# Optimization experiments

Hardware: AMD Instinct MI355X
Metric: run time of the kernel (lower is better)

The kernel has to match this reference:

```python
import jax, jax.numpy as jnp
import numpy as np

N, C, NELL, NSPEC = 4096, 128, 9, 10
K3, K2, K1 = 4, 2, 1
IRREPS_OUT = (("0e", 1), ("1o", 3))  # keep_irrep_out dims


def setup_inputs() -> dict:
    key = jax.random.key(0)
    ks = iter(jax.random.split(key, 32))

    def rn(shape, scale=1.0):
        return jax.random.normal(next(ks), shape, jnp.float32) * jnp.float32(scale)

    inp = {}
    inp["x"] = rn((N, C, NELL))
    inp["node_specie"] = jax.random.randint(next(ks), (N,), 0, NSPEC)
    for name, d in IRREPS_OUT:
        # CG symmetric-product basis tensors (fixed buffers), normalized per order
        inp[f"U3_{name}"] = rn((d, NELL, NELL, NELL, K3), 1.0 / np.sqrt(NELL ** 3))
        inp[f"U2_{name}"] = rn((d, NELL, NELL, K2), 1.0 / np.sqrt(NELL ** 2))
        inp[f"U1_{name}"] = rn((d, NELL, K1), 1.0 / np.sqrt(NELL))
        # per-species path-mixing weights, 'element' gradient normalization ~ 1/sqrt(k)
        inp[f"W3_{name}"] = rn((NSPEC, K3, C), 1.0 / np.sqrt(K3))
        inp[f"W2_{name}"] = rn((NSPEC, K2, C), 1.0 / np.sqrt(K2))
        inp[f"W1_{name}"] = rn((NSPEC, K1, C), 1.0 / np.sqrt(K1))
    inp["Wlin_0e"] = rn((C, C))
    inp["Wlin_1o"] = rn((C, C))
    inp["bias_0e"] = rn((C,), 0.1)
    return inp


def _symmetric_contraction(x, specie, U3, U2, U1, W3, W2, W1):
    # MACE iterative contraction: out = U3.W3.x; then (U2.W2 + out).x; then (U1.W1 + out).x
    w3, w2, w1 = W3[specie], W2[specie], W1[specie]  # (N, k, C)
    out = jnp.einsum("opqik,bkc,bci->bcopq", U3, w3, x)   # (N, C, d, 9, 9)
    c = jnp.einsum("opik,bkc->bcopi", U2, w2) + out
    out = jnp.einsum("bcopi,bci->bcop", c, x)             # (N, C, d, 9)
    c = jnp.einsum("oik,bkc->bcoi", U1, w1) + out
    out = jnp.einsum("bcoi,bci->bco", c, x)               # (N, C, d)
    return out


def reference(x, node_specie,
              U3_0e, U2_0e, U1_0e, W3_0e, W2_0e, W1_0e,
              U3_1o, U2_1o, U1_1o, W3_1o, W2_1o, W1_1o,
              Wlin_0e, Wlin_1o, bias_0e):
    n = x.shape[0]
    f0 = _symmetric_contraction(x, node_specie, U3_0e, U2_0e, U1_0e, W3_0e, W2_0e, W1_0e)  # (N, C, 1)
    f1 = _symmetric_contraction(x, node_specie, U3_1o, U2_1o, U1_1o, W3_1o, W2_1o, W1_1o)  # (N, C, 3)
    scale = jnp.float32(1.0 / np.sqrt(C))  # e3nn Linear path normalization
    y0 = jnp.einsum("nco,cm->nmo", f0, Wlin_0e) * scale + bias_0e[None, :, None]  # bias only on 0e
    y1 = jnp.einsum("nco,cm->nmo", f1, Wlin_1o) * scale
    # axis_to_mul: flatten (channels, ir_dim) per irrep and concatenate
    return jnp.concatenate([y0.reshape(n, -1), y1.reshape(n, -1)], axis=-1)  # (N, 128*1 + 128*3)
```

## Files before the change

### kernel.cpp

```cpp
#include <hip/hip_runtime.h>

#define N_NODES 4096
#define C_CH    128
#define NSPEC   10
#define NCUB    165
#define NQUAD   45
#define NMONO   219
#define NBLK    1280
#define NTILE   8

#define WS_CNT    0
#define WS_LIST   256
#define WS_U3SYM  164096
#define WS_U2SYM  174656
#define WS_COEFF  176096
#define WS_F      4661216

__global__ void k_prep(const float* __restrict__ U3_0e, const float* __restrict__ U3_1o,
                       const float* __restrict__ U2_0e, const float* __restrict__ U2_1o,
                       int* __restrict__ cnt, float* __restrict__ U3sym,
                       float* __restrict__ U2sym) {
    __shared__ unsigned char ta[NCUB], tb[NCUB], td[NCUB], qa[NQUAD], qb[NQUAD];
    int t = threadIdx.x;
    if (t < NSPEC) cnt[t] = 0;
    if (t < NCUB) {
        int idx = 0, a = 0, b = 0, d = 0;
        for (int a0 = 0; a0 < 9; a0++)
            for (int b0 = a0; b0 < 9; b0++)
                for (int d0 = b0; d0 < 9; d0++) {
                    if (idx == t) { a = a0; b = b0; d = d0; }
                    idx++;
                }
        ta[t] = a; tb[t] = b; td[t] = d;
    } else if (t >= 256 && t < 256 + NQUAD) {
        int q = t - 256, idx = 0, a = 0, b = 0;
        for (int a0 = 0; a0 < 9; a0++)
            for (int b0 = a0; b0 < 9; b0++) { if (idx == q) { a = a0; b = b0; } idx++; }
        qa[q] = a; qb[q] = b;
    }
    __syncthreads();
    for (int task = t; task < 2640 + 360; task += blockDim.x) {
        if (task < 2640) {
            int og = task / 660;
            int r  = task - og * 660;
            int m  = r >> 2, k = r & 3;
            int a = ta[m], b = tb[m], d = td[m];
            const float* U3 = (og == 0) ? U3_0e : U3_1o;
            int o = (og == 0) ? 0 : og - 1;
            const float* Ub = U3 + (size_t)o * 2916;
            #define U3AT(p,q,i) Ub[((p)*9+(q))*36 + (i)*4 + k]
            float sum = U3AT(a,b,d) + U3AT(a,d,b) + U3AT(b,a,d)
                      + U3AT(b,d,a) + U3AT(d,a,b) + U3AT(d,b,a);
            #undef U3AT
            float sc = (a == b && b == d) ? (1.f/6.f)
                     : ((a == b || b == d || a == d) ? 0.5f : 1.f);
            U3sym[(og * 165 + m) * 4 + k] = sum * sc;
        } else {
            int t2 = task - 2640;
            int og = t2 / 90;
            int r  = t2 - og * 90;
            int q  = r >> 1, k = r & 1;
            int a = qa[q], b = qb[q];
            const float* U2 = (og == 0) ? U2_0e : U2_1o;
            int o = (og == 0) ? 0 : og - 1;
            const float* Ub = U2 + (size_t)o * 162;
            float sum = Ub[(a*9 + b)*2 + k] + Ub[(b*9 + a)*2 + k];
            if (a == b) sum *= 0.5f;
            U2sym[(og * 45 + q) * 2 + k] = sum;
        }
    }
}

__global__ void k_lists(const int* __restrict__ specie, int* __restrict__ cnt,
                        int* __restrict__ list) {
    int i = blockIdx.x * blockDim.x + threadIdx.x;
    if (i < N_NODES) {
        int s = specie[i];
        int pos = atomicAdd(&cnt[s], 1);
        list[s * N_NODES + pos] = i;
    }
}

__global__ void k_coeff(const float* __restrict__ U3sym, const float* __restrict__ U2sym,
                        const float* __restrict__ U1_0e, const float* __restrict__ U1_1o,
                        const float* __restrict__ W3_0e, const float* __restrict__ W3_1o,
                        const float* __restrict__ W2_0e, const float* __restrict__ W2_1o,
                        const float* __restrict__ W1_0e, const float* __restrict__ W1_1o,
                        float* __restrict__ coeff) {
    int blk = blockIdx.x;
    int s = blk >> 7, c = blk & 127;
    int t = threadIdx.x;
    if (t >= NMONO * 4) return;
    int m = t >> 2, og = t & 3;
    float val;
    if (m < NCUB) {
        const float* W3 = (og == 0) ? W3_0e : W3_1o;
        const float* u  = U3sym + (og * 165 + m) * 4;
        val = u[0] * W3[s*512 +       c] + u[1] * W3[s*512 + 128 + c]
            + u[2] * W3[s*512 + 256 + c] + u[3] * W3[s*512 + 384 + c];
    } else if (m < NCUB + NQUAD) {
        int q = m - NCUB;
        const float* W2 = (og == 0) ? W2_0e : W2_1o;
        const float* u  = U2sym + (og * 45 + q) * 2;
        val = u[0] * W2[s*256 + c] + u[1] * W2[s*256 + 128 + c];
    } else {
        int l = m - (NCUB + NQUAD);
        const float* U1 = (og == 0) ? U1_0e : U1_1o;
        const float* W1 = (og == 0) ? W1_0e : W1_1o;
        int o = (og == 0) ? 0 : og - 1;
        val = U1[o * 9 + l] * W1[s * 128 + c];
    }
    coeff[(size_t)blk * (NMONO * 4) + t] = val;
}

__global__ __launch_bounds__(256) void k_main(const float* __restrict__ x,
        const int* __restrict__ cnt, const int* __restrict__ list,
        const float* __restrict__ coeff, float* __restrict__ fout) {
    __shared__ float  cfs[NMONO * 4];
    __shared__ float2 xsh[9 * 256];
    int bx   = blockIdx.x;
    int tile = bx / NBLK;
    int blk  = bx - tile * NBLK;
    int s = blk >> 7, c = blk & 127;
    int n = cnt[s];
    if (tile * 512 >= n) return;

    int tid = threadIdx.x;
    if (tid < NMONO)
        ((float4*)cfs)[tid] =
            ((const float4*)(coeff + (size_t)blk * (NMONO * 4)))[tid];

    const int* __restrict__ lst = list + s * N_NODES;
    int i0 = tile * 512 + tid;
    int i1 = i0 + 256;
    int b0 = lst[i0 < n ? i0 : 0];
    int b1 = lst[i1 < n ? i1 : 0];
    const float* xp0 = x + ((size_t)b0 * C_CH + c) * 9;
    const float* xp1 = x + ((size_t)b1 * C_CH + c) * 9;
    #pragma unroll
    for (int i = 0; i < 9; i++)
        xsh[i * 256 + tid] = make_float2(xp0[i], xp1[i]);
    __syncthreads();

    float a0[4] = {0.f, 0.f, 0.f, 0.f};
    float a1[4] = {0.f, 0.f, 0.f, 0.f};
    int mcub = 0, mquad = 0;

    #pragma unroll 1
    for (int a = 0; a < 9; a++) {
        float2 xa = xsh[a * 256 + tid];
        {
            float4 cl = *(const float4*)&cfs[(210 + a) * 4];
            a0[0] = fmaf(cl.x, xa.x, a0[0]);  a1[0] = fmaf(cl.x, xa.y, a1[0]);
            a0[1] = fmaf(cl.y, xa.x, a0[1]);  a1[1] = fmaf(cl.y, xa.y, a1[1]);
            a0[2] = fmaf(cl.z, xa.x, a0[2]);  a1[2] = fmaf(cl.z, xa.y, a1[2]);
            a0[3] = fmaf(cl.w, xa.x, a0[3]);  a1[3] = fmaf(cl.w, xa.y, a1[3]);
        }
        #pragma unroll 1
        for (int b = a; b < 9; b++) {
            float2 xb = xsh[b * 256 + tid];
            float p0 = xa.x * xb.x, p1 = xa.y * xb.y;
            {
                float4 cq = *(const float4*)&cfs[(165 + mquad) * 4]; mquad++;
                a0[0] = fmaf(cq.x, p0, a0[0]);  a1[0] = fmaf(cq.x, p1, a1[0]);
                a0[1] = fmaf(cq.y, p0, a0[1]);  a1[1] = fmaf(cq.y, p1, a1[1]);
                a0[2] = fmaf(cq.z, p0, a0[2]);  a1[2] = fmaf(cq.z, p1, a1[2]);
                a0[3] = fmaf(cq.w, p0, a0[3]);  a1[3] = fmaf(cq.w, p1, a1[3]);
            }
            #pragma unroll 1
            for (int d = b; d < 9; d++) {
                float2 xd = xsh[d * 256 + tid];
                float4 c3 = *(const float4*)&cfs[mcub * 4]; mcub++;
                float q0 = p0 * xd.x, q1 = p1 * xd.y;
                a0[0] = fmaf(c3.x, q0, a0[0]);  a1[0] = fmaf(c3.x, q1, a1[0]);
                a0[1] = fmaf(c3.y, q0, a0[1]);  a1[1] = fmaf(c3.y, q1, a1[1]);
                a0[2] = fmaf(c3.z, q0, a0[2]);  a1[2] = fmaf(c3.z, q1, a1[2]);
                a0[3] = fmaf(c3.w, q0, a0[3]);  a1[3] = fmaf(c3.w, q1, a1[3]);
            }
        }
    }
    if (i0 < n) *(float4*)&fout[((size_t)b0 * C_CH + c) * 4] = make_float4(a0[0], a0[1], a0[2], a0[3]);
    if (i1 < n) *(float4*)&fout[((size_t)b1 * C_CH + c) * 4] = make_float4(a1[0], a1[1], a1[2], a1[3]);
}

__global__ __launch_bounds__(256) void k_epi(const float* __restrict__ f,
        const float* __restrict__ W0, const float* __restrict__ W1,
        const float* __restrict__ bias, float* __restrict__ out) {
    __shared__ float smem[128 * 65];
    int bx = blockIdx.x;
    int ntile = bx >> 3, jg = bx & 7;
    int n0 = ntile * 64;
    int t  = threadIdx.x;
    int o  = jg >> 1;

    #pragma unroll
    for (int r = 0; r < 32; ++r) {
        int flat = r * 256 + t;
        int n = flat >> 7, c = flat & 127;
        smem[c * 65 + n] = f[(size_t)(n0 + n) * 512 + c * 4 + o];
    }
    __syncthreads();

    int w    = __builtin_amdgcn_readfirstlane((int)(t >> 6));
    int lane = t & 63;
    int mb   = (jg & 1) * 64 + w * 16;
    const float* __restrict__ Wsel = (o == 0) ? W0 : W1;

    float acc[16];
    #pragma unroll
    for (int jj = 0; jj < 16; jj++) acc[jj] = 0.f;

    #pragma unroll 4
    for (int c = 0; c < 128; ++c) {
        float fv = smem[c * 65 + lane];
        #pragma unroll
        for (int jj = 0; jj < 16; jj++)
            acc[jj] = fmaf(fv, Wsel[c * 128 + mb + jj], acc[jj]);
    }
    __syncthreads();

    const float scale = 0.08838834764831845f;
    #pragma unroll
    for (int jj = 0; jj < 16; jj++) {
        float v = acc[jj] * scale;
        if (o == 0) v += bias[mb + jj];
        smem[(w * 16 + jj) * 65 + lane] = v;
    }
    __syncthreads();

    #pragma unroll
    for (int r = 0; r < 16; ++r) {
        int flat = r * 256 + t;
        int jl = flat & 63, n = flat >> 6;
        int m  = (jg & 1) * 64 + jl;
        int col = (o == 0) ? m : (128 + m * 3 + (o - 1));
        out[(size_t)(n0 + n) * 512 + col] = smem[jl * 65 + n];
    }
}

extern "C" void kernel_launch(void* const* d_in, const int* in_sizes, int n_in,
                              void* d_out, int out_size, void* d_ws, size_t ws_size,
                              hipStream_t stream) {
    const float* x     = (const float*)d_in[0];
    const int*   spec  = (const int*)  d_in[1];
    const float* U3_0e = (const float*)d_in[2];
    const float* U2_0e = (const float*)d_in[3];
    const float* U1_0e = (const float*)d_in[4];
    const float* W3_0e = (const float*)d_in[5];
    const float* W2_0e = (const float*)d_in[6];
    const float* W1_0e = (const float*)d_in[7];
    const float* U3_1o = (const float*)d_in[8];
    const float* U2_1o = (const float*)d_in[9];
    const float* U1_1o = (const float*)d_in[10];
    const float* W3_1o = (const float*)d_in[11];
    const float* W2_1o = (const float*)d_in[12];
    const float* W1_1o = (const float*)d_in[13];
    const float* Wlin0 = (const float*)d_in[14];
    const float* Wlin1 = (const float*)d_in[15];
    const float* bias0 = (const float*)d_in[16];
    float* out = (float*)d_out;

    char* ws = (char*)d_ws;
    int*   cnt   = (int*)  (ws + WS_CNT);
    int*   list  = (int*)  (ws + WS_LIST);
    float* U3sym = (float*)(ws + WS_U3SYM);
    float* U2sym = (float*)(ws + WS_U2SYM);
    float* coeff = (float*)(ws + WS_COEFF);
    float* f     = (float*)(ws + WS_F);
    (void)in_sizes; (void)n_in; (void)out_size; (void)ws_size;

    hipLaunchKernelGGL(k_prep,  dim3(1),    dim3(1024), 0, stream,
                       U3_0e, U3_1o, U2_0e, U2_1o, cnt, U3sym, U2sym);
    hipLaunchKernelGGL(k_lists, dim3(16),   dim3(256),  0, stream, spec, cnt, list);
    hipLaunchKernelGGL(k_coeff, dim3(1280), dim3(896),  0, stream,
                       U3sym, U2sym, U1_0e, U1_1o, W3_0e, W3_1o,
                       W2_0e, W2_1o, W1_0e, W1_1o, coeff);
    hipLaunchKernelGGL(k_main,  dim3(NBLK * NTILE), dim3(256), 0, stream,
                       x, cnt, list, coeff, f);
    hipLaunchKernelGGL(k_epi,   dim3(512),  dim3(256),  0, stream, f, Wlin0, Wlin1, bias0, out);
}
```

Baseline: 185.2 us.

## Fuse list building into prep and compute coefficients inside main kernel

Merges the species-list kernel into a multi-block prep kernel: one block builds the per-species node lists with shared-memory atomics, and eight blocks compute the symmetrized U tensors. The per-(species, channel) coefficient kernel and its workspace buffer are removed, and k_main now computes its 876 coefficients directly into shared memory. This drops two launches and a roughly 4.5 MB coefficient write and read-back. In exchange, every main block, including tiles that are only partly filled, recomputes its coefficients from global U and W buffers.

```diff
diff --git a/kernel.cpp b/kernel.cpp
--- a/kernel.cpp
+++ b/kernel.cpp
@@ -13,16 +13,32 @@
 #define WS_LIST   256
 #define WS_U3SYM  164096
 #define WS_U2SYM  174656
-#define WS_COEFF  176096
-#define WS_F      4661216
-
-__global__ void k_prep(const float* __restrict__ U3_0e, const float* __restrict__ U3_1o,
-                       const float* __restrict__ U2_0e, const float* __restrict__ U2_1o,
-                       int* __restrict__ cnt, float* __restrict__ U3sym,
-                       float* __restrict__ U2sym) {
+#define WS_F      176096
+
+__global__ __launch_bounds__(256) void k_prep(
+        const float* __restrict__ U3_0e, const float* __restrict__ U3_1o,
+        const float* __restrict__ U2_0e, const float* __restrict__ U2_1o,
+        const int* __restrict__ specie, int* __restrict__ cnt,
+        int* __restrict__ list, float* __restrict__ U3sym,
+        float* __restrict__ U2sym) {
+    int blk = blockIdx.x;
+    int t   = threadIdx.x;
+
+    if (blk == 8) {
+        __shared__ int scnt[NSPEC];
+        if (t < NSPEC) scnt[t] = 0;
+        __syncthreads();
+        for (int i = t; i < N_NODES; i += 256) {
+            int s = specie[i];
+            int pos = atomicAdd(&scnt[s], 1);
+            list[s * N_NODES + pos] = i;
+        }
+        __syncthreads();
+        if (t < NSPEC) cnt[t] = scnt[t];
+        return;
+    }
+
     __shared__ unsigned char ta[NCUB], tb[NCUB], td[NCUB], qa[NQUAD], qb[NQUAD];
-    int t = threadIdx.x;
-    if (t < NSPEC) cnt[t] = 0;
     if (t < NCUB) {
         int idx = 0, a = 0, b = 0, d = 0;
         for (int a0 = 0; a0 < 9; a0++)
@@ -32,14 +48,15 @@
                     idx++;
                 }
         ta[t] = a; tb[t] = b; td[t] = d;
-    } else if (t >= 256 && t < 256 + NQUAD) {
-        int q = t - 256, idx = 0, a = 0, b = 0;
+    } else if (t >= NCUB && t < NCUB + NQUAD) {
+        int q = t - NCUB, idx = 0, a = 0, b = 0;
         for (int a0 = 0; a0 < 9; a0++)
             for (int b0 = a0; b0 < 9; b0++) { if (idx == q) { a = a0; b = b0; } idx++; }
         qa[q] = a; qb[q] = b;
     }
     __syncthreads();
-    for (int task = t; task < 2640 + 360; task += blockDim.x) {
+
+    for (int task = blk * 256 + t; task < 2640 + 360; task += 8 * 256) {
         if (task < 2640) {
             int og = task / 660;
             int r  = task - og * 660;
@@ -71,51 +88,14 @@
     }
 }
 
-__global__ void k_lists(const int* __restrict__ specie, int* __restrict__ cnt,
-                        int* __restrict__ list) {
-    int i = blockIdx.x * blockDim.x + threadIdx.x;
-    if (i < N_NODES) {
-        int s = specie[i];
-        int pos = atomicAdd(&cnt[s], 1);
-        list[s * N_NODES + pos] = i;
-    }
-}
-
-__global__ void k_coeff(const float* __restrict__ U3sym, const float* __restrict__ U2sym,
-                        const float* __restrict__ U1_0e, const float* __restrict__ U1_1o,
-                        const float* __restrict__ W3_0e, const float* __restrict__ W3_1o,
-                        const float* __restrict__ W2_0e, const float* __restrict__ W2_1o,
-                        const float* __restrict__ W1_0e, const float* __restrict__ W1_1o,
-                        float* __restrict__ coeff) {
-    int blk = blockIdx.x;
-    int s = blk >> 7, c = blk & 127;
-    int t = threadIdx.x;
-    if (t >= NMONO * 4) return;
-    int m = t >> 2, og = t & 3;
-    float val;
-    if (m < NCUB) {
-        const float* W3 = (og == 0) ? W3_0e : W3_1o;
-        const float* u  = U3sym + (og * 165 + m) * 4;
-        val = u[0] * W3[s*512 +       c] + u[1] * W3[s*512 + 128 + c]
-            + u[2] * W3[s*512 + 256 + c] + u[3] * W3[s*512 + 384 + c];
-    } else if (m < NCUB + NQUAD) {
-        int q = m - NCUB;
-        const float* W2 = (og == 0) ? W2_0e : W2_1o;
-        const float* u  = U2sym + (og * 45 + q) * 2;
-        val = u[0] * W2[s*256 + c] + u[1] * W2[s*256 + 128 + c];
-    } else {
-        int l = m - (NCUB + NQUAD);
-        const float* U1 = (og == 0) ? U1_0e : U1_1o;
-        const float* W1 = (og == 0) ? W1_0e : W1_1o;
-        int o = (og == 0) ? 0 : og - 1;
-        val = U1[o * 9 + l] * W1[s * 128 + c];
-    }
-    coeff[(size_t)blk * (NMONO * 4) + t] = val;
-}
-
 __global__ __launch_bounds__(256) void k_main(const float* __restrict__ x,
         const int* __restrict__ cnt, const int* __restrict__ list,
-        const float* __restrict__ coeff, float* __restrict__ fout) {
+        const float* __restrict__ U3sym, const float* __restrict__ U2sym,
+        const float* __restrict__ U1_0e, const float* __restrict__ U1_1o,
+        const float* __restrict__ W3_0e, const float* __restrict__ W3_1o,
+        const float* __restrict__ W2_0e, const float* __restrict__ W2_1o,
+        const float* __restrict__ W1_0e, const float* __restrict__ W1_1o,
+        float* __restrict__ fout) {
     __shared__ float  cfs[NMONO * 4];
     __shared__ float2 xsh[9 * 256];
     int bx   = blockIdx.x;
@@ -126,9 +106,29 @@
     if (tile * 512 >= n) return;
 
     int tid = threadIdx.x;
-    if (tid < NMONO)
-        ((float4*)cfs)[tid] =
-            ((const float4*)(coeff + (size_t)blk * (NMONO * 4)))[tid];
+
+    for (int e = tid; e < NMONO * 4; e += 256) {
+        int m = e >> 2, og = e & 3;
+        float val;
+        if (m < NCUB) {
+            const float* W3 = (og == 0) ? W3_0e : W3_1o;
+            const float* u  = U3sym + (og * 165 + m) * 4;
+            val = u[0] * W3[s*512 +       c] + u[1] * W3[s*512 + 128 + c]
+                + u[2] * W3[s*512 + 256 + c] + u[3] * W3[s*512 + 384 + c];
+        } else if (m < NCUB + NQUAD) {
+            int q = m - NCUB;
+            const float* W2 = (og == 0) ? W2_0e : W2_1o;
+            const float* u  = U2sym + (og * 45 + q) * 2;
+            val = u[0] * W2[s*256 + c] + u[1] * W2[s*256 + 128 + c];
+        } else {
+            int l = m - (NCUB + NQUAD);
+            const float* U1 = (og == 0) ? U1_0e : U1_1o;
+            const float* W1 = (og == 0) ? W1_0e : W1_1o;
+            int o = (og == 0) ? 0 : og - 1;
+            val = U1[o * 9 + l] * W1[s * 128 + c];
+        }
+        cfs[e] = val;
+    }
 
     const int* __restrict__ lst = list + s * N_NODES;
     int i0 = tile * 512 + tid;
@@ -265,17 +265,14 @@
     int*   list  = (int*)  (ws + WS_LIST);
     float* U3sym = (float*)(ws + WS_U3SYM);
     float* U2sym = (float*)(ws + WS_U2SYM);
-    float* coeff = (float*)(ws + WS_COEFF);
     float* f     = (float*)(ws + WS_F);
     (void)in_sizes; (void)n_in; (void)out_size; (void)ws_size;
 
-    hipLaunchKernelGGL(k_prep,  dim3(1),    dim3(1024), 0, stream,
-                       U3_0e, U3_1o, U2_0e, U2_1o, cnt, U3sym, U2sym);
-    hipLaunchKernelGGL(k_lists, dim3(16),   dim3(256),  0, stream, spec, cnt, list);
-    hipLaunchKernelGGL(k_coeff, dim3(1280), dim3(896),  0, stream,
-                       U3sym, U2sym, U1_0e, U1_1o, W3_0e, W3_1o,
-                       W2_0e, W2_1o, W1_0e, W1_1o, coeff);
-    hipLaunchKernelGGL(k_main,  dim3(NBLK * NTILE), dim3(256), 0, stream,
-                       x, cnt, list, coeff, f);
-    hipLaunchKernelGGL(k_epi,   dim3(512),  dim3(256),  0, stream, f, Wlin0, Wlin1, bias0, out);
-}
+    hipLaunchKernelGGL(k_prep, dim3(9), dim3(256), 0, stream,
+                       U3_0e, U3_1o, U2_0e, U2_1o, spec, cnt, list, U3sym, U2sym);
+    hipLaunchKernelGGL(k_main, dim3(NBLK * NTILE), dim3(256), 0, stream,
+                       x, cnt, list, U3sym, U2sym, U1_0e, U1_1o,
+                       W3_0e, W3_1o, W2_0e, W2_1o, W1_0e, W1_1o, f);
+    hipLaunchKernelGGL(k_epi, dim3(512), dim3(256), 0, stream,
+                       f, Wlin0, Wlin1, bias0, out);
+}
```

Measured after the change: 165.2 us. 1.12x faster.
